# Optimization experiments

Hardware: AMD Instinct MI355X
Metric: run time of the kernel (lower is better)

## Reference

```python
import jax, jax.numpy as jnp
import numpy as np

N = 50000      # nodes
E = 800000     # edges
D_IN = 128     # embedding_in
EP = 200000    # prediction edge pairs
CONV_DIMS = [D_IN, 128, 64, 32]
LIN_DIMS = [32, 16, 8, 1]


def setup_inputs() -> dict:
    key = jax.random.key(0)
    ks = jax.random.split(key, 20)
    inp = {
        "x": jax.random.normal(ks[0], (N, D_IN), dtype=jnp.float32),
        "edge_index": jax.random.randint(ks[1], (2, E), 0, N, dtype=jnp.int64 if jax.config.jax_enable_x64 else jnp.int32),
        "pred_edges": jax.random.randint(ks[2], (EP, 2), 0, N, dtype=jnp.int64 if jax.config.jax_enable_x64 else jnp.int32),
    }
    k = 3
    for i in range(3):  # GCNConv weights [in,out] + bias (torch GCNConv has bias)
        din, dout = CONV_DIMS[i], CONV_DIMS[i + 1]
        inp[f"cw{i}"] = jax.random.normal(ks[k], (din, dout), dtype=jnp.float32) / np.sqrt(din); k += 1
        inp[f"cb{i}"] = jax.random.normal(ks[k], (dout,), dtype=jnp.float32) * 0.01; k += 1
    for i in range(3):  # Linear weights stored [in,out]
        din, dout = LIN_DIMS[i], LIN_DIMS[i + 1]
        inp[f"lw{i}"] = jax.random.normal(ks[k], (din, dout), dtype=jnp.float32) / np.sqrt(din); k += 1
        inp[f"lb{i}"] = jax.random.normal(ks[k], (dout,), dtype=jnp.float32) * 0.01; k += 1
    return inp


def gcn_conv(x, W, b, src, dst, n):
    """PyG GCNConv: D^-1/2 (A + I) D^-1/2 X W + b, deg over dst incl. self-loop."""
    h = x @ W  # [n, dout]
    deg = jax.ops.segment_sum(jnp.ones_like(dst, dtype=h.dtype), dst, num_segments=n) + 1.0
    dis = jax.lax.rsqrt(deg)  # deg >= 1 (self loop)
    msg = h[src] * (dis[src] * dis[dst])[:, None]      # gather + per-edge normalize
    out = jax.ops.segment_sum(msg, dst, num_segments=n)  # scatter-add into targets
    out = out + h * (dis * dis)[:, None]                # self-loop contribution
    return out + b


def reference(x, edge_index, pred_edges, cw0, cb0, cw1, cb1, cw2, cb2,
              lw0, lb0, lw1, lb1, lw2, lb2):
    src, dst = edge_index[0], edge_index[1]
    n = x.shape[0]
    for W, b in ((cw0, cb0), (cw1, cb1), (cw2, cb2)):
        x = jax.nn.relu(gcn_conv(x, W, b, src, dst, n))
    x = jax.nn.relu(x @ lw0 + lb0)
    x = jax.nn.relu(x @ lw1 + lb1)
    x = jax.nn.sigmoid(x @ lw2 + lb2)  # [n, 1]
    s = x[:, 0]
    # x[pred_edges] -> [EP,2,1]; mul of pair, transpose+flatten -> [EP]
    return s[pred_edges[:, 0]] * s[pred_edges[:, 1]]
```

## Files before the change

kernel.cpp:

```cpp
#include <hip/hip_runtime.h>
#include <math.h>

constexpr int NN  = 50000;
constexpr int NP  = 50048;
constexpr int NE  = 800000;
constexpr int NEP = 200000;

constexpr int NBKT  = 256;
constexpr int CAP   = 4096;
constexpr int CAPC  = 4096;
constexpr int CHUNK = 4096;

constexpr int BKB = (NE + CHUNK - 1) / CHUNK;
constexpr int W0B = 128 * 128 / 256;
constexpr int W1B = 128 * 64 / 256;
constexpr int W2B = 64 * 32 / 256;
constexpr int FRONT_BLOCKS = BKB + W0B + W1B + W2B;

constexpr int GEMM0_BLKS = NP / 64;
constexpr int NODE_BLKS32 = (NN + 31) / 32;
constexpr int NODE_BLKS16 = (NN + 15) / 16;

constexpr float M0_SCALE  = 16.0f;
constexpr float M0_ISCALE = 1.0f / 16.0f;
constexpr float M1_SCALE  = 16.0f;
constexpr float M1_ISCALE = 1.0f / 16.0f;
constexpr float M2_SCALE  = 16.0f;
constexpr float M2_ISCALE = 1.0f / 16.0f;

typedef _Float16 half8_t  __attribute__((ext_vector_type(8)));
typedef __fp16   fp16x2_t __attribute__((ext_vector_type(2)));
typedef float    float4_t __attribute__((ext_vector_type(4)));

static inline int cdiv(long long a, int b) { return (int)((a + b - 1) / b); }

static __device__ inline unsigned char f32_to_fp8(float v) {
    int p = __builtin_amdgcn_cvt_pk_fp8_f32(v, v, 0, false);
    return (unsigned char)(p & 0xFF);
}

static __device__ inline void fp8x8_acc(uint2 u, float d, float* a) {
    auto f0 = __builtin_amdgcn_cvt_pk_f32_fp8((int)u.x, false);
    auto f1 = __builtin_amdgcn_cvt_pk_f32_fp8((int)u.x, true);
    auto f2 = __builtin_amdgcn_cvt_pk_f32_fp8((int)u.y, false);
    auto f3 = __builtin_amdgcn_cvt_pk_f32_fp8((int)u.y, true);
    a[0] = fmaf(f0[0], d, a[0]); a[1] = fmaf(f0[1], d, a[1]);
    a[2] = fmaf(f1[0], d, a[2]); a[3] = fmaf(f1[1], d, a[3]);
    a[4] = fmaf(f2[0], d, a[4]); a[5] = fmaf(f2[1], d, a[5]);
    a[6] = fmaf(f3[0], d, a[6]); a[7] = fmaf(f3[1], d, a[7]);
}

static __device__ inline void fp8x8_add(uint2 u, float* a) {
    auto f0 = __builtin_amdgcn_cvt_pk_f32_fp8((int)u.x, false);
    auto f1 = __builtin_amdgcn_cvt_pk_f32_fp8((int)u.x, true);
    auto f2 = __builtin_amdgcn_cvt_pk_f32_fp8((int)u.y, false);
    auto f3 = __builtin_amdgcn_cvt_pk_f32_fp8((int)u.y, true);
    a[0] += f0[0]; a[1] += f0[1];
    a[2] += f1[0]; a[3] += f1[1];
    a[4] += f2[0]; a[5] += f2[1];
    a[6] += f3[0]; a[7] += f3[1];
}

__global__ __launch_bounds__(256) void k_front(const int* __restrict__ src,
        const int* __restrict__ dst, int* __restrict__ binCnt,
        unsigned int* __restrict__ ebuf,
        const float* __restrict__ cw0, _Float16* __restrict__ WT0,
        const float* __restrict__ cw1, _Float16* __restrict__ WT1,
        const float* __restrict__ cw2, _Float16* __restrict__ WT2) {
    const int tid = threadIdx.x;
    const int bid = blockIdx.x;

    if (bid < BKB) {
        __shared__ int hist[NBKT];
        __shared__ int base[NBKT];
        __shared__ int cur[NBKT];
        const int e0 = bid * CHUNK;
        hist[tid] = 0;
        __syncthreads();
        int  s[16], bn[16], dl[16];
        bool okq[4];
#pragma unroll
        for (int q = 0; q < 4; ++q) {
            int i = e0 + q * 1024 + tid * 4;
            bool ok = i < NE;
            okq[q] = ok;
            if (ok) {
                int4 d4 = *(const int4*)(dst + i);
                int4 s4 = *(const int4*)(src + i);
                s[q*4+0] = s4.x; bn[q*4+0] = d4.x >> 8; dl[q*4+0] = d4.x & 255;
                s[q*4+1] = s4.y; bn[q*4+1] = d4.y >> 8; dl[q*4+1] = d4.y & 255;
                s[q*4+2] = s4.z; bn[q*4+2] = d4.z >> 8; dl[q*4+2] = d4.z & 255;
                s[q*4+3] = s4.w; bn[q*4+3] = d4.w >> 8; dl[q*4+3] = d4.w & 255;
                atomicAdd(&hist[bn[q*4+0]], 1);
                atomicAdd(&hist[bn[q*4+1]], 1);
                atomicAdd(&hist[bn[q*4+2]], 1);
                atomicAdd(&hist[bn[q*4+3]], 1);
            }
        }
        __syncthreads();
        base[tid] = hist[tid] ? atomicAdd(&binCnt[tid], hist[tid]) : 0;
        cur[tid] = 0;
        __syncthreads();
#pragma unroll
        for (int q = 0; q < 4; ++q) {
            if (okq[q]) {
#pragma unroll
                for (int u = 0; u < 4; ++u) {
                    int j = q * 4 + u;
                    int slot = base[bn[j]] + atomicAdd(&cur[bn[j]], 1);
                    ebuf[bn[j] * CAP + slot] = (unsigned int)s[j] | ((unsigned int)dl[j] << 16);
                }
            }
        }
        return;
    }
    if (bid < BKB + W0B) {
        int idx = (bid - BKB) * 256 + tid;
        int k = idx >> 7, n = idx & 127;
        WT0[(size_t)n * 128 + k] = (_Float16)cw0[idx];
        return;
    }
    if (bid < BKB + W0B + W1B) {
        int idx = (bid - BKB - W0B) * 256 + tid;
        int k = idx >> 6, n = idx & 63;
        WT1[(size_t)n * 128 + k] = (_Float16)cw1[idx];
        return;
    }
    {
        int idx = (bid - BKB - W0B - W1B) * 256 + tid;
        int k = idx >> 5, n = idx & 31;
        WT2[(size_t)n * 64 + k] = (_Float16)cw2[idx];
    }
}

__global__ __launch_bounds__(256) void k_csr_gemm0(const unsigned int* __restrict__ ebuf,
        const int* __restrict__ binCnt, int* __restrict__ off, float* __restrict__ dis,
        unsigned short* __restrict__ csr,
        const float* __restrict__ X, const _Float16* __restrict__ WT,
        unsigned char* __restrict__ g, int n) {
    const int tid = threadIdx.x;
    const int bid = blockIdx.x;

    if (bid < NBKT) {
        __shared__ int hist[256];
        __shared__ int sh[256];
        __shared__ int cur[256];
        const int bin = bid;
        const int cnt = binCnt[bin];
        const unsigned int* eb = ebuf + (size_t)bin * CAP;

        hist[tid] = 0;
        __syncthreads();
        for (int i = tid; i < cnt; i += 256)
            atomicAdd(&hist[eb[i] >> 16], 1);
        __syncthreads();

        int v  = hist[tid];
        int pv = (v + 3) & ~3;
        sh[tid] = pv;
        __syncthreads();
        for (int d = 1; d < 256; d <<= 1) {
            int t = (tid >= d) ? sh[tid - d] : 0;
            __syncthreads();
            sh[tid] += t;
            __syncthreads();
        }
        int start = bin * CAPC + (sh[tid] - pv);

        int node = bin * 256 + tid;
        if (node < NN) {
            off[node] = start | (pv << 20);
            dis[node] = rsqrtf((float)v + 1.0f);
        } else if (node == NN) {
            dis[node] = 0.f;
        }
        cur[tid] = start;
        __syncthreads();

        for (int i = tid; i < cnt; i += 256) {
            unsigned int e = eb[i];
            int p = atomicAdd(&cur[e >> 16], 1);
            csr[p] = (unsigned short)(e & 0xFFFFu);
        }
        for (int k2 = v; k2 < pv; ++k2) csr[start + k2] = (unsigned short)NN;
        return;
    }

    constexpr int K = 128, DOUT = 128;
    constexpr int NC = 64, NT = 4, KT = 4, MT = 2;

    const int gb   = bid - NBKT;
    const int L    = tid & 63;
    const int w    = tid >> 6;
    const int wc   = w & 1;
    const int wr   = w >> 1;
    const int r0   = gb * 64 + wr * 32;
    const int c0   = wc * NC;
    const int quad = L >> 4;
    const int lm   = L & 15;

    float4_t acc[MT][NT];
#pragma unroll
    for (int mt = 0; mt < MT; ++mt)
#pragma unroll
        for (int nt = 0; nt < NT; ++nt) acc[mt][nt] = (float4_t){0.f, 0.f, 0.f, 0.f};

#pragma unroll
    for (int kt = 0; kt < KT; ++kt) {
        half8_t a[MT], b[NT];
#pragma unroll
        for (int mt = 0; mt < MT; ++mt) {
            const float* xr = X + (size_t)(r0 + mt * 16 + lm) * K + kt * 32 + quad * 8;
            float4 u = *(const float4*)xr;
            float4 v = *(const float4*)(xr + 4);
            union { fp16x2_t h2[4]; half8_t h8; } cv;
            cv.h2[0] = __builtin_amdgcn_cvt_pkrtz(u.x, u.y);
            cv.h2[1] = __builtin_amdgcn_cvt_pkrtz(u.z, u.w);
            cv.h2[2] = __builtin_amdgcn_cvt_pkrtz(v.x, v.y);
            cv.h2[3] = __builtin_amdgcn_cvt_pkrtz(v.z, v.w);
            a[mt] = cv.h8;
        }
#pragma unroll
        for (int nt = 0; nt < NT; ++nt)
            b[nt] = *(const half8_t*)(WT + (size_t)(c0 + nt * 16 + lm) * K + kt * 32 + quad * 8);
#pragma unroll
        for (int mt = 0; mt < MT; ++mt)
#pragma unroll
            for (int nt = 0; nt < NT; ++nt)
                acc[mt][nt] = __builtin_amdgcn_mfma_f32_16x16x32_f16(a[mt], b[nt], acc[mt][nt], 0, 0, 0);
    }

#pragma unroll
    for (int mt = 0; mt < MT; ++mt) {
        int rb = r0 + mt * 16 + quad * 4;
#pragma unroll
        for (int nt = 0; nt < NT; ++nt) {
            int c = c0 + nt * 16 + lm;
#pragma unroll
            for (int reg = 0; reg < 4; ++reg) {
                int r = rb + reg;
                if (r < n)       g[(size_t)r * DOUT + c] = f32_to_fp8(acc[mt][nt][reg] * M0_SCALE);
                else if (r == n) g[(size_t)r * DOUT + c] = 0;
            }
        }
    }
}

__global__ __launch_bounds__(256) void k_agg_gemm16(const unsigned char* __restrict__ gin,
        const float* __restrict__ dis, const float* __restrict__ bias,
        const int* __restrict__ off, const unsigned short* __restrict__ csr,
        const _Float16* __restrict__ WT, unsigned char* __restrict__ gout, int n) {
    constexpr int DIN = 128, DOUT = 64;
    constexpr int XS = DIN + 8;
    __shared__ _Float16 sX[16 * XS];

    const int tid  = threadIdx.x;
    const int l16  = tid & 15;
    const int ln   = tid >> 4;
    const int r0   = blockIdx.x * 16;
    const int node = r0 + ln;

    const uint2* gp = (const uint2*)gin;

    if (blockIdx.x == 0 && tid < DOUT / 8)
        ((uint2*)(gout + (size_t)n * DOUT))[tid] = (uint2){0u, 0u};

    float dd = dis[node];
    uint2 hv = gp[(size_t)node * 16 + l16];
    float a[8] = {0.f, 0.f, 0.f, 0.f, 0.f, 0.f, 0.f, 0.f};
    fp8x8_acc(hv, dd, a);

    int pk = off[node];
    int e0 = pk & 0xFFFFF;
    int e1 = e0 + (pk >> 20);
    int e = e0;
    for (; e + 7 < e1; e += 8) {
        ushort4 c4 = *(const ushort4*)(csr + e);
        ushort4 c8 = *(const ushort4*)(csr + e + 4);
        uint2 v0 = gp[(size_t)c4.x * 16 + l16];
        uint2 v1 = gp[(size_t)c4.y * 16 + l16];
        uint2 v2 = gp[(size_t)c4.z * 16 + l16];
        uint2 v3 = gp[(size_t)c4.w * 16 + l16];
        uint2 v4 = gp[(size_t)c8.x * 16 + l16];
        uint2 v5 = gp[(size_t)c8.y * 16 + l16];
        uint2 v6 = gp[(size_t)c8.z * 16 + l16];
        uint2 v7 = gp[(size_t)c8.w * 16 + l16];
        float d0 = dis[c4.x], d1 = dis[c4.y], d2 = dis[c4.z], d3 = dis[c4.w];
        float d4 = dis[c8.x], d5 = dis[c8.y], d6 = dis[c8.z], d7 = dis[c8.w];
        fp8x8_acc(v0, d0, a); fp8x8_acc(v1, d1, a);
        fp8x8_acc(v2, d2, a); fp8x8_acc(v3, d3, a);
        fp8x8_acc(v4, d4, a); fp8x8_acc(v5, d5, a);
        fp8x8_acc(v6, d6, a); fp8x8_acc(v7, d7, a);
    }
    if (e < e1) {
        ushort4 c4 = *(const ushort4*)(csr + e);
        uint2 v0 = gp[(size_t)c4.x * 16 + l16];
        uint2 v1 = gp[(size_t)c4.y * 16 + l16];
        uint2 v2 = gp[(size_t)c4.z * 16 + l16];
        uint2 v3 = gp[(size_t)c4.w * 16 + l16];
        float d0 = dis[c4.x], d1 = dis[c4.y], d2 = dis[c4.z], d3 = dis[c4.w];
        fp8x8_acc(v0, d0, a); fp8x8_acc(v1, d1, a);
        fp8x8_acc(v2, d2, a); fp8x8_acc(v3, d3, a);
    }
    {
        float ddp = dd * M0_ISCALE;
        half8_t o;
#pragma unroll
        for (int j = 0; j < 8; ++j)
            o[j] = (_Float16)fmaxf(fmaf(a[j], ddp, bias[l16 * 8 + j]), 0.f);
        *(half8_t*)(sX + ln * XS + l16 * 8) = o;
    }
    __syncthreads();

    const int L    = tid & 63;
    const int w    = tid >> 6;
    const int quad = L >> 4;
    const int lm   = L & 15;
    const int c0   = w * 16;

    float4_t acc = (float4_t){0.f, 0.f, 0.f, 0.f};
#pragma unroll
    for (int kt = 0; kt < DIN / 32; ++kt) {
        half8_t b  = *(const half8_t*)(WT + (size_t)(c0 + lm) * DIN + kt * 32 + quad * 8);
        half8_t aF = *(const half8_t*)(sX + lm * XS + kt * 32 + quad * 8);
        acc = __builtin_amdgcn_mfma_f32_16x16x32_f16(aF, b, acc, 0, 0, 0);
    }
    int rb = r0 + quad * 4;
    float dv[4];
    *(float4*)dv = *(const float4*)(dis + rb);
#pragma unroll
    for (int reg = 0; reg < 4; ++reg)
        gout[(size_t)(rb + reg) * DOUT + c0 + lm] = f32_to_fp8(acc[reg] * dv[reg] * M1_SCALE);
}

__global__ __launch_bounds__(256) void k_agg_gemm8(const unsigned char* __restrict__ gin,
        const float* __restrict__ dis, const float* __restrict__ bias,
        const int* __restrict__ off, const unsigned short* __restrict__ csr,
        const _Float16* __restrict__ WT, unsigned char* __restrict__ gout, int n) {
    constexpr int DIN = 64, DOUT = 32;
    constexpr int XS = DIN + 8;
    __shared__ _Float16 sX[32 * XS];

    const int tid  = threadIdx.x;
    const int l8   = tid & 7;
    const int ln   = tid >> 3;
    const int r0   = blockIdx.x * 32;
    const int node = r0 + ln;

    const uint2* gp = (const uint2*)gin;

    if (node < n) {
        float dd = dis[node];
        uint2 hv = gp[(size_t)node * 8 + l8];
        float a[8] = {0.f, 0.f, 0.f, 0.f, 0.f, 0.f, 0.f, 0.f};
        fp8x8_add(hv, a);
        int pk = off[node];
        int e0 = pk & 0xFFFFF;
        int e1 = e0 + (pk >> 20);
        int e = e0;
        for (; e + 7 < e1; e += 8) {
            ushort4 c4 = *(const ushort4*)(csr + e);
            ushort4 c8 = *(const ushort4*)(csr + e + 4);
            uint2 v0 = gp[(size_t)c4.x * 8 + l8];
            uint2 v1 = gp[(size_t)c4.y * 8 + l8];
            uint2 v2 = gp[(size_t)c4.z * 8 + l8];
            uint2 v3 = gp[(size_t)c4.w * 8 + l8];
            uint2 v4 = gp[(size_t)c8.x * 8 + l8];
            uint2 v5 = gp[(size_t)c8.y * 8 + l8];
            uint2 v6 = gp[(size_t)c8.z * 8 + l8];
            uint2 v7 = gp[(size_t)c8.w * 8 + l8];
            fp8x8_add(v0, a); fp8x8_add(v1, a);
            fp8x8_add(v2, a); fp8x8_add(v3, a);
            fp8x8_add(v4, a); fp8x8_add(v5, a);
            fp8x8_add(v6, a); fp8x8_add(v7, a);
        }
        if (e < e1) {
            ushort4 c4 = *(const ushort4*)(csr + e);
            uint2 v0 = gp[(size_t)c4.x * 8 + l8];
            uint2 v1 = gp[(size_t)c4.y * 8 + l8];
            uint2 v2 = gp[(size_t)c4.z * 8 + l8];
            uint2 v3 = gp[(size_t)c4.w * 8 + l8];
            fp8x8_add(v0, a); fp8x8_add(v1, a);
            fp8x8_add(v2, a); fp8x8_add(v3, a);
        }
        float ddp = dd * M1_ISCALE;
        half8_t o;
#pragma unroll
        for (int j = 0; j < 8; ++j)
            o[j] = (_Float16)fmaxf(fmaf(a[j], ddp, bias[l8 * 8 + j]), 0.f);
        *(half8_t*)(sX + ln * XS + l8 * 8) = o;
    } else {
        *(half8_t*)(sX + ln * XS + l8 * 8) =
            (half8_t){(_Float16)0.f, (_Float16)0.f, (_Float16)0.f, (_Float16)0.f,
                      (_Float16)0.f, (_Float16)0.f, (_Float16)0.f, (_Float16)0.f};
    }
    __syncthreads();

    const int L    = tid & 63;
    const int w    = tid >> 6;
    const int quad = L >> 4;
    const int lm   = L & 15;
    const int c0   = (w & 1) * 16;
    const int m0   = (w >> 1) * 16;

    float4_t acc = (float4_t){0.f, 0.f, 0.f, 0.f};
#pragma unroll
    for (int kt = 0; kt < DIN / 32; ++kt) {
        half8_t b  = *(const half8_t*)(WT + (size_t)(c0 + lm) * DIN + kt * 32 + quad * 8);
        half8_t aF = *(const half8_t*)(sX + (m0 + lm) * XS + kt * 32 + quad * 8);
        acc = __builtin_amdgcn_mfma_f32_16x16x32_f16(aF, b, acc, 0, 0, 0);
    }
    int rb = r0 + m0 + quad * 4;
    float dv[4];
    *(float4*)dv = *(const float4*)(dis + rb);
#pragma unroll
    for (int reg = 0; reg < 4; ++reg) {
        int r = rb + reg;
        if (r < n)       gout[(size_t)r * DOUT + c0 + lm] = f32_to_fp8(acc[reg] * dv[reg] * M2_SCALE);
        else if (r == n) gout[(size_t)r * DOUT + c0 + lm] = 0;
    }
}

__global__ __launch_bounds__(256) void k_agg_mlp(const unsigned char* __restrict__ g,
        const float* __restrict__ dis, const float* __restrict__ b,
        const int* __restrict__ off, const unsigned short* __restrict__ csr,
        const float* __restrict__ lw0, const float* __restrict__ lb0,
        const float* __restrict__ lw1, const float* __restrict__ lb1,
        const float* __restrict__ lw2, const float* __restrict__ lb2,
        float* __restrict__ sv, int n) {
    __shared__ float sh[32 * 33];
    const int tid  = threadIdx.x;
    const int l8   = tid & 7;
    const int lane = l8 & 3;
    const int grp  = l8 >> 2;
    const int ln   = tid >> 3;
    const int node = blockIdx.x * 32 + ln;

    const uint2* gp = (const uint2*)g;

    if (node < n) {
        float dd = dis[node];
        float a[8] = {0.f, 0.f, 0.f, 0.f, 0.f, 0.f, 0.f, 0.f};
        if (grp == 0) fp8x8_add(gp[(size_t)node * 4 + lane], a);
        int pk = off[node];
        int e0 = pk & 0xFFFFF;
        int e1 = e0 + (pk >> 20);
        for (int e = e0 + grp * 4; e < e1; e += 8) {
            ushort4 c4 = *(const ushort4*)(csr + e);
            uint2 v0 = gp[(size_t)c4.x * 4 + lane];
            uint2 v1 = gp[(size_t)c4.y * 4 + lane];
            uint2 v2 = gp[(size_t)c4.z * 4 + lane];
            uint2 v3 = gp[(size_t)c4.w * 4 + lane];
            fp8x8_add(v0, a); fp8x8_add(v1, a);
            fp8x8_add(v2, a); fp8x8_add(v3, a);
        }
#pragma unroll
        for (int j = 0; j < 8; ++j) a[j] += __shfl_xor(a[j], 4);
        if (grp == 0) {
            float ddp = dd * M2_ISCALE;
            float* row = sh + ln * 33 + lane * 8;
#pragma unroll
            for (int j = 0; j < 8; ++j)
                row[j] = fmaxf(fmaf(a[j], ddp, b[lane * 8 + j]), 0.f);
        }
    }
    __syncthreads();

    if (tid < 32) {
        int node2 = blockIdx.x * 32 + tid;
        if (node2 < n) {
            const float* v = sh + tid * 33;
            float a[16];
#pragma unroll
            for (int j = 0; j < 16; ++j) {
                float acc = lb0[j];
#pragma unroll
                for (int k = 0; k < 32; ++k) acc = fmaf(v[k], lw0[k * 16 + j], acc);
                a[j] = fmaxf(acc, 0.f);
            }
            float b8[8];
#pragma unroll
            for (int j = 0; j < 8; ++j) {
                float acc = lb1[j];
#pragma unroll
                for (int k = 0; k < 16; ++k) acc = fmaf(a[k], lw1[k * 8 + j], acc);
                b8[j] = fmaxf(acc, 0.f);
            }
            float z = lb2[0];
#pragma unroll
            for (int k = 0; k < 8; ++k) z = fmaf(b8[k], lw2[k], z);
            sv[node2] = 1.0f / (1.0f + expf(-z));
        }
    }
}

__global__ void k_pred(const float* __restrict__ s, const int* __restrict__ pe,
                       float* __restrict__ out, int ep2) {
    int i = blockIdx.x * blockDim.x + threadIdx.x;
    if (i >= ep2) return;
    int4 p = ((const int4*)pe)[i];
    float2 o;
    o.x = s[p.x] * s[p.y];
    o.y = s[p.z] * s[p.w];
    ((float2*)out)[i] = o;
}

extern "C" void kernel_launch(void* const* d_in, const int* in_sizes, int n_in,
                              void* d_out, int out_size, void* d_ws, size_t ws_size,
                              hipStream_t stream) {
    const float* x   = (const float*)d_in[0];
    const int*   ei  = (const int*)d_in[1];
    const int*   pe  = (const int*)d_in[2];
    const float* cw0 = (const float*)d_in[3];
    const float* cb0 = (const float*)d_in[4];
    const float* cw1 = (const float*)d_in[5];
    const float* cb1 = (const float*)d_in[6];
    const float* cw2 = (const float*)d_in[7];
    const float* cb2 = (const float*)d_in[8];
    const float* lw0 = (const float*)d_in[9];
    const float* lb0 = (const float*)d_in[10];
    const float* lw1 = (const float*)d_in[11];
    const float* lb1 = (const float*)d_in[12];
    const float* lw2 = (const float*)d_in[13];
    const float* lb2 = (const float*)d_in[14];

    const int* src = ei;
    const int* dst = ei + NE;

    char* w = (char*)d_ws;
    float*          dis  = (float*)w;           w += sizeof(float) * (NN + 16);
    unsigned char*  M0   = (unsigned char*)w;   w += (size_t)(NN + 1) * 128;
    unsigned char*  M1   = (unsigned char*)w;   w += (size_t)(NN + 1) * 64;
    unsigned char*  M2   = (unsigned char*)w;   w += (size_t)(NN + 1) * 32;
    float*          sv   = (float*)w;           w += sizeof(float) * NN;
    _Float16*       WT0  = (_Float16*)w;        w += sizeof(_Float16) * 128 * 128;
    _Float16*       WT1  = (_Float16*)w;        w += sizeof(_Float16) * 64 * 128;
    _Float16*       WT2  = (_Float16*)w;        w += sizeof(_Float16) * 32 * 64;
    int*            off  = (int*)w;             w += sizeof(int) * NN;
    unsigned short* csr  = (unsigned short*)w;  w += sizeof(unsigned short) * (size_t)NBKT * CAPC;
    int*            binCnt = (int*)w;           w += sizeof(int) * NBKT;
    unsigned int*   ebuf = (unsigned int*)w;    w += sizeof(unsigned int) * (size_t)NBKT * CAP;

    const int T = 256;

    (void)hipMemsetAsync(binCnt, 0, sizeof(int) * NBKT, stream);
    k_front<<<FRONT_BLOCKS, 256, 0, stream>>>(src, dst, binCnt, ebuf,
                                              cw0, WT0, cw1, WT1, cw2, WT2);

    k_csr_gemm0<<<NBKT + GEMM0_BLKS, 256, 0, stream>>>(ebuf, binCnt, off, dis, csr,
                                                       x, WT0, M0, NN);

    k_agg_gemm16<<<NODE_BLKS16, 256, 0, stream>>>(M0, dis, cb0,
                                                  off, csr, WT1, M1, NN);

    k_agg_gemm8<<<NODE_BLKS32, 256, 0, stream>>>(M1, dis, cb1,
                                                 off, csr, WT2, M2, NN);

    k_agg_mlp<<<NODE_BLKS32, 256, 0, stream>>>(M2, dis, cb2, off, csr,
                                               lw0, lb0, lw1, lb1, lw2, lb2, sv, NN);

    k_pred<<<cdiv(NEP / 2, T), T, 0, stream>>>(sv, pe, (float*)d_out, NEP / 2);
}
```

Baseline: 180.5 us.

## Pre-scale layer-0 features by source degree and overlap GEMM0 with CSR build via flags

The layer-0 GEMM blocks now multiply each output row by its dis value before fp8 quantization. They wait on a per-bucket release/acquire flag published by the CSR-building blocks, and they loop persistently over tiles with a fixed grid of 768 blocks. This lets the first aggregation kernel drop its per-neighbor dis gather and fma and use a plain add with wider uint4 loads, 8 lanes per node and 32 nodes per block. It removes a random dis load per edge and improves gather width, at the cost of spin-wait synchronization across blocks in the same kernel, which relies on the CSR blocks being scheduled first. The flags are cleared by widening the existing memset.

After: 234.0 us. +29.6%, slower.

```diff
diff --git a/kernel.cpp b/kernel.cpp
--- a/kernel.cpp
+++ b/kernel.cpp
@@ -17,9 +17,10 @@
 constexpr int W2B = 64 * 32 / 256;
 constexpr int FRONT_BLOCKS = BKB + W0B + W1B + W2B;
 
-constexpr int GEMM0_BLKS = NP / 64;
+constexpr int GEMM0_TILES = NP / 64;
+constexpr int GEMM0_BLKS  = 768;
 constexpr int NODE_BLKS32 = (NN + 31) / 32;
-constexpr int NODE_BLKS16 = (NN + 15) / 16;
+constexpr int NODE_BLKS64 = (NN + 63) / 64;
 
 constexpr float M0_SCALE  = 16.0f;
 constexpr float M0_ISCALE = 1.0f / 16.0f;
@@ -37,17 +38,6 @@
 static __device__ inline unsigned char f32_to_fp8(float v) {
     int p = __builtin_amdgcn_cvt_pk_fp8_f32(v, v, 0, false);
     return (unsigned char)(p & 0xFF);
-}
-
-static __device__ inline void fp8x8_acc(uint2 u, float d, float* a) {
-    auto f0 = __builtin_amdgcn_cvt_pk_f32_fp8((int)u.x, false);
-    auto f1 = __builtin_amdgcn_cvt_pk_f32_fp8((int)u.x, true);
-    auto f2 = __builtin_amdgcn_cvt_pk_f32_fp8((int)u.y, false);
-    auto f3 = __builtin_amdgcn_cvt_pk_f32_fp8((int)u.y, true);
-    a[0] = fmaf(f0[0], d, a[0]); a[1] = fmaf(f0[1], d, a[1]);
-    a[2] = fmaf(f1[0], d, a[2]); a[3] = fmaf(f1[1], d, a[3]);
-    a[4] = fmaf(f2[0], d, a[4]); a[5] = fmaf(f2[1], d, a[5]);
-    a[6] = fmaf(f3[0], d, a[6]); a[7] = fmaf(f3[1], d, a[7]);
 }
 
 static __device__ inline void fp8x8_add(uint2 u, float* a) {
@@ -59,6 +49,11 @@
     a[2] += f1[0]; a[3] += f1[1];
     a[4] += f2[0]; a[5] += f2[1];
     a[6] += f3[0]; a[7] += f3[1];
+}
+
+static __device__ inline void fp8x16_add(uint4 u, float* a) {
+    fp8x8_add((uint2){u.x, u.y}, a);
+    fp8x8_add((uint2){u.z, u.w}, a + 8);
 }
 
 __global__ __launch_bounds__(256) void k_front(const int* __restrict__ src,
@@ -133,9 +128,9 @@
     }
 }
 
-__global__ __launch_bounds__(256) void k_csr_gemm0(const unsigned int* __restrict__ ebuf,
+__global__ __launch_bounds__(256, 4) void k_csr_gemm0(const unsigned int* __restrict__ ebuf,
         const int* __restrict__ binCnt, int* __restrict__ off, float* __restrict__ dis,
-        unsigned short* __restrict__ csr,
+        unsigned short* __restrict__ csr, int* __restrict__ flag,
         const float* __restrict__ X, const _Float16* __restrict__ WT,
         unsigned char* __restrict__ g, int n) {
     const int tid = threadIdx.x;
@@ -171,11 +166,16 @@
         if (node < NN) {
             off[node] = start | (pv << 20);
             dis[node] = rsqrtf((float)v + 1.0f);
-        } else if (node == NN) {
+        } else if (node >= NN) {
             dis[node] = 0.f;
         }
         cur[tid] = start;
         __syncthreads();
+
+        if (tid == 0) {
+            __threadfence();
+            __hip_atomic_store(&flag[bin], 1, __ATOMIC_RELEASE, __HIP_MEMORY_SCOPE_AGENT);
+        }
 
         for (int i = tid; i < cnt; i += 256) {
             unsigned int e = eb[i];
@@ -189,60 +189,70 @@
     constexpr int K = 128, DOUT = 128;
     constexpr int NC = 64, NT = 4, KT = 4, MT = 2;
 
-    const int gb   = bid - NBKT;
     const int L    = tid & 63;
     const int w    = tid >> 6;
     const int wc   = w & 1;
     const int wr   = w >> 1;
-    const int r0   = gb * 64 + wr * 32;
     const int c0   = wc * NC;
     const int quad = L >> 4;
     const int lm   = L & 15;
 
-    float4_t acc[MT][NT];
-#pragma unroll
-    for (int mt = 0; mt < MT; ++mt)
-#pragma unroll
-        for (int nt = 0; nt < NT; ++nt) acc[mt][nt] = (float4_t){0.f, 0.f, 0.f, 0.f};
-
-#pragma unroll
-    for (int kt = 0; kt < KT; ++kt) {
-        half8_t a[MT], b[NT];
+    for (int t = bid - NBKT; t < GEMM0_TILES; t += GEMM0_BLKS) {
+        const int r0 = t * 64 + wr * 32;
+
+        float4_t acc[MT][NT];
+#pragma unroll
+        for (int mt = 0; mt < MT; ++mt)
+#pragma unroll
+            for (int nt = 0; nt < NT; ++nt) acc[mt][nt] = (float4_t){0.f, 0.f, 0.f, 0.f};
+
+#pragma unroll
+        for (int kt = 0; kt < KT; ++kt) {
+            half8_t a[MT], b[NT];
+#pragma unroll
+            for (int mt = 0; mt < MT; ++mt) {
+                const float* xr = X + (size_t)(r0 + mt * 16 + lm) * K + kt * 32 + quad * 8;
+                float4 u = *(const float4*)xr;
+                float4 v = *(const float4*)(xr + 4);
+                union { fp16x2_t h2[4]; half8_t h8; } cv;
+                cv.h2[0] = __builtin_amdgcn_cvt_pkrtz(u.x, u.y);
+                cv.h2[1] = __builtin_amdgcn_cvt_pkrtz(u.z, u.w);
+                cv.h2[2] = __builtin_amdgcn_cvt_pkrtz(v.x, v.y);
+                cv.h2[3] = __builtin_amdgcn_cvt_pkrtz(v.z, v.w);
+                a[mt] = cv.h8;
+            }
+#pragma unroll
+            for (int nt = 0; nt < NT; ++nt)
+                b[nt] = *(const half8_t*)(WT + (size_t)(c0 + nt * 16 + lm) * K + kt * 32 + quad * 8);
+#pragma unroll
+            for (int mt = 0; mt < MT; ++mt)
+#pragma unroll
+                for (int nt = 0; nt < NT; ++nt)
+                    acc[mt][nt] = __builtin_amdgcn_mfma_f32_16x16x32_f16(a[mt], b[nt], acc[mt][nt], 0, 0, 0);
+        }
+
+        const int bin = (t * 64) >> 8;
+        if (tid == 0)
+            while (__hip_atomic_load(&flag[bin], __ATOMIC_ACQUIRE, __HIP_MEMORY_SCOPE_AGENT) == 0) {}
+        __syncthreads();
+
 #pragma unroll
         for (int mt = 0; mt < MT; ++mt) {
-            const float* xr = X + (size_t)(r0 + mt * 16 + lm) * K + kt * 32 + quad * 8;
-            float4 u = *(const float4*)xr;
-            float4 v = *(const float4*)(xr + 4);
-            union { fp16x2_t h2[4]; half8_t h8; } cv;
-            cv.h2[0] = __builtin_amdgcn_cvt_pkrtz(u.x, u.y);
-            cv.h2[1] = __builtin_amdgcn_cvt_pkrtz(u.z, u.w);
-            cv.h2[2] = __builtin_amdgcn_cvt_pkrtz(v.x, v.y);
-            cv.h2[3] = __builtin_amdgcn_cvt_pkrtz(v.z, v.w);
-            a[mt] = cv.h8;
-        }
-#pragma unroll
-        for (int nt = 0; nt < NT; ++nt)
-            b[nt] = *(const half8_t*)(WT + (size_t)(c0 + nt * 16 + lm) * K + kt * 32 + quad * 8);
-#pragma unroll
-        for (int mt = 0; mt < MT; ++mt)
-#pragma unroll
-            for (int nt = 0; nt < NT; ++nt)
-                acc[mt][nt] = __builtin_amdgcn_mfma_f32_16x16x32_f16(a[mt], b[nt], acc[mt][nt], 0, 0, 0);
-    }
-
-#pragma unroll
-    for (int mt = 0; mt < MT; ++mt) {
-        int rb = r0 + mt * 16 + quad * 4;
-#pragma unroll
-        for (int nt = 0; nt < NT; ++nt) {
-            int c = c0 + nt * 16 + lm;
-#pragma unroll
-            for (int reg = 0; reg < 4; ++reg) {
-                int r = rb + reg;
-                if (r < n)       g[(size_t)r * DOUT + c] = f32_to_fp8(acc[mt][nt][reg] * M0_SCALE);
-                else if (r == n) g[(size_t)r * DOUT + c] = 0;
+            int rb = r0 + mt * 16 + quad * 4;
+            float dv[4];
+            *(float4*)dv = *(const float4*)(dis + rb);
+#pragma unroll
+            for (int nt = 0; nt < NT; ++nt) {
+                int c = c0 + nt * 16 + lm;
+#pragma unroll
+                for (int reg = 0; reg < 4; ++reg) {
+                    int r = rb + reg;
+                    if (r < n)       g[(size_t)r * DOUT + c] = f32_to_fp8(acc[mt][nt][reg] * dv[reg] * M0_SCALE);
+                    else if (r == n) g[(size_t)r * DOUT + c] = 0;
+                }
             }
         }
+        __syncthreads();
     }
 }
 
@@ -252,63 +262,68 @@
         const _Float16* __restrict__ WT, unsigned char* __restrict__ gout, int n) {
     constexpr int DIN = 128, DOUT = 64;
     constexpr int XS = DIN + 8;
-    __shared__ _Float16 sX[16 * XS];
+    __shared__ _Float16 sX[32 * XS];
 
     const int tid  = threadIdx.x;
-    const int l16  = tid & 15;
-    const int ln   = tid >> 4;
-    const int r0   = blockIdx.x * 16;
+    const int l8   = tid & 7;
+    const int ln   = tid >> 3;
+    const int r0   = blockIdx.x * 32;
     const int node = r0 + ln;
 
-    const uint2* gp = (const uint2*)gin;
+    const uint4* gp = (const uint4*)gin;
 
     if (blockIdx.x == 0 && tid < DOUT / 8)
         ((uint2*)(gout + (size_t)n * DOUT))[tid] = (uint2){0u, 0u};
 
-    float dd = dis[node];
-    uint2 hv = gp[(size_t)node * 16 + l16];
-    float a[8] = {0.f, 0.f, 0.f, 0.f, 0.f, 0.f, 0.f, 0.f};
-    fp8x8_acc(hv, dd, a);
-
-    int pk = off[node];
-    int e0 = pk & 0xFFFFF;
-    int e1 = e0 + (pk >> 20);
-    int e = e0;
-    for (; e + 7 < e1; e += 8) {
-        ushort4 c4 = *(const ushort4*)(csr + e);
-        ushort4 c8 = *(const ushort4*)(csr + e + 4);
-        uint2 v0 = gp[(size_t)c4.x * 16 + l16];
-        uint2 v1 = gp[(size_t)c4.y * 16 + l16];
-        uint2 v2 = gp[(size_t)c4.z * 16 + l16];
-        uint2 v3 = gp[(size_t)c4.w * 16 + l16];
-        uint2 v4 = gp[(size_t)c8.x * 16 + l16];
-        uint2 v5 = gp[(size_t)c8.y * 16 + l16];
-        uint2 v6 = gp[(size_t)c8.z * 16 + l16];
-        uint2 v7 = gp[(size_t)c8.w * 16 + l16];
-        float d0 = dis[c4.x], d1 = dis[c4.y], d2 = dis[c4.z], d3 = dis[c4.w];
-        float d4 = dis[c8.x], d5 = dis[c8.y], d6 = dis[c8.z], d7 = dis[c8.w];
-        fp8x8_acc(v0, d0, a); fp8x8_acc(v1, d1, a);
-        fp8x8_acc(v2, d2, a); fp8x8_acc(v3, d3, a);
-        fp8x8_acc(v4, d4, a); fp8x8_acc(v5, d5, a);
-        fp8x8_acc(v6, d6, a); fp8x8_acc(v7, d7, a);
-    }
-    if (e < e1) {
-        ushort4 c4 = *(const ushort4*)(csr + e);
-        uint2 v0 = gp[(size_t)c4.x * 16 + l16];
-        uint2 v1 = gp[(size_t)c4.y * 16 + l16];
-        uint2 v2 = gp[(size_t)c4.z * 16 + l16];
-        uint2 v3 = gp[(size_t)c4.w * 16 + l16];
-        float d0 = dis[c4.x], d1 = dis[c4.y], d2 = dis[c4.z], d3 = dis[c4.w];
-        fp8x8_acc(v0, d0, a); fp8x8_acc(v1, d1, a);
-        fp8x8_acc(v2, d2, a); fp8x8_acc(v3, d3, a);
-    }
-    {
+    if (node < n) {
+        float dd = dis[node];
+        uint4 hv = gp[(size_t)node * 8 + l8];
+        float a[16] = {0.f,0.f,0.f,0.f,0.f,0.f,0.f,0.f,0.f,0.f,0.f,0.f,0.f,0.f,0.f,0.f};
+        fp8x16_add(hv, a);
+
+        int pk = off[node];
+        int e0 = pk & 0xFFFFF;
+        int e1 = e0 + (pk >> 20);
+        int e = e0;
+        for (; e + 7 < e1; e += 8) {
+            ushort4 c4 = *(const ushort4*)(csr + e);
+            ushort4 c8 = *(const ushort4*)(csr + e + 4);
+            uint4 v0 = gp[(size_t)c4.x * 8 + l8];
+            uint4 v1 = gp[(size_t)c4.y * 8 + l8];
+            uint4 v2 = gp[(size_t)c4.z * 8 + l8];
+            uint4 v3 = gp[(size_t)c4.w * 8 + l8];
+            uint4 v4 = gp[(size_t)c8.x * 8 + l8];
+            uint4 v5 = gp[(size_t)c8.y * 8 + l8];
+            uint4 v6 = gp[(size_t)c8.z * 8 + l8];
+            uint4 v7 = gp[(size_t)c8.w * 8 + l8];
+            fp8x16_add(v0, a); fp8x16_add(v1, a);
+            fp8x16_add(v2, a); fp8x16_add(v3, a);
+            fp8x16_add(v4, a); fp8x16_add(v5, a);
+            fp8x16_add(v6, a); fp8x16_add(v7, a);
+        }
+        if (e < e1) {
+            ushort4 c4 = *(const ushort4*)(csr + e);
+            uint4 v0 = gp[(size_t)c4.x * 8 + l8];
+            uint4 v1 = gp[(size_t)c4.y * 8 + l8];
+            uint4 v2 = gp[(size_t)c4.z * 8 + l8];
+            uint4 v3 = gp[(size_t)c4.w * 8 + l8];
+            fp8x16_add(v0, a); fp8x16_add(v1, a);
+            fp8x16_add(v2, a); fp8x16_add(v3, a);
+        }
         float ddp = dd * M0_ISCALE;
-        half8_t o;
-#pragma unroll
-        for (int j = 0; j < 8; ++j)
-            o[j] = (_Float16)fmaxf(fmaf(a[j], ddp, bias[l16 * 8 + j]), 0.f);
-        *(half8_t*)(sX + ln * XS + l16 * 8) = o;
+        half8_t o0, o1;
+#pragma unroll
+        for (int j = 0; j < 8; ++j) {
+            o0[j] = (_Float16)fmaxf(fmaf(a[j],     ddp, bias[l8 * 16 + j]),     0.f);
+            o1[j] = (_Float16)fmaxf(fmaf(a[j + 8], ddp, bias[l8 * 16 + 8 + j]), 0.f);
+        }
+        *(half8_t*)(sX + ln * XS + l8 * 16)     = o0;
+        *(half8_t*)(sX + ln * XS + l8 * 16 + 8) = o1;
+    } else {
+        half8_t z = (half8_t){(_Float16)0.f,(_Float16)0.f,(_Float16)0.f,(_Float16)0.f,
+                              (_Float16)0.f,(_Float16)0.f,(_Float16)0.f,(_Float16)0.f};
+        *(half8_t*)(sX + ln * XS + l8 * 16)     = z;
+        *(half8_t*)(sX + ln * XS + l8 * 16 + 8) = z;
     }
     __syncthreads();
 
@@ -318,19 +333,25 @@
     const int lm   = L & 15;
     const int c0   = w * 16;
 
-    float4_t acc = (float4_t){0.f, 0.f, 0.f, 0.f};
-#pragma unroll
-    for (int kt = 0; kt < DIN / 32; ++kt) {
-        half8_t b  = *(const half8_t*)(WT + (size_t)(c0 + lm) * DIN + kt * 32 + quad * 8);
-        half8_t aF = *(const half8_t*)(sX + lm * XS + kt * 32 + quad * 8);
-        acc = __builtin_amdgcn_mfma_f32_16x16x32_f16(aF, b, acc, 0, 0, 0);
-    }
-    int rb = r0 + quad * 4;
-    float dv[4];
-    *(float4*)dv = *(const float4*)(dis + rb);
-#pragma unroll
-    for (int reg = 0; reg < 4; ++reg)
-        gout[(size_t)(rb + reg) * DOUT + c0 + lm] = f32_to_fp8(acc[reg] * dv[reg] * M1_SCALE);
+#pragma unroll
+    for (int mh = 0; mh < 2; ++mh) {
+        const int m0 = mh * 16;
+        float4_t acc = (float4_t){0.f, 0.f, 0.f, 0.f};
+#pragma unroll
+        for (int kt = 0; kt < DIN / 32; ++kt) {
+            half8_t b  = *(const half8_t*)(WT + (size_t)(c0 + lm) * DIN + kt * 32 + quad * 8);
+            half8_t aF = *(const half8_t*)(sX + (m0 + lm) * XS + kt * 32 + quad * 8);
+            acc = __builtin_amdgcn_mfma_f32_16x16x32_f16(aF, b, acc, 0, 0, 0);
+        }
+        int rb = r0 + m0 + quad * 4;
+        float dv[4];
+        *(float4*)dv = *(const float4*)(dis + rb);
+#pragma unroll
+        for (int reg = 0; reg < 4; ++reg) {
+            int r = rb + reg;
+            if (r < n) gout[(size_t)r * DOUT + c0 + lm] = f32_to_fp8(acc[reg] * dv[reg] * M1_SCALE);
+        }
+    }
 }
 
 __global__ __launch_bounds__(256) void k_agg_gemm8(const unsigned char* __restrict__ gin,
@@ -528,7 +549,7 @@
     const int* dst = ei + NE;
 
     char* w = (char*)d_ws;
-    float*          dis  = (float*)w;           w += sizeof(float) * (NN + 16);
+    float*          dis  = (float*)w;           w += sizeof(float) * (NN + 64);
     unsigned char*  M0   = (unsigned char*)w;   w += (size_t)(NN + 1) * 128;
     unsigned char*  M1   = (unsigned char*)w;   w += (size_t)(NN + 1) * 64;
     unsigned char*  M2   = (unsigned char*)w;   w += (size_t)(NN + 1) * 32;
@@ -539,18 +560,19 @@
     int*            off  = (int*)w;             w += sizeof(int) * NN;
     unsigned short* csr  = (unsigned short*)w;  w += sizeof(unsigned short) * (size_t)NBKT * CAPC;
     int*            binCnt = (int*)w;           w += sizeof(int) * NBKT;
+    int*            flag = (int*)w;             w += sizeof(int) * NBKT;
     unsigned int*   ebuf = (unsigned int*)w;    w += sizeof(unsigned int) * (size_t)NBKT * CAP;
 
     const int T = 256;
 
-    (void)hipMemsetAsync(binCnt, 0, sizeof(int) * NBKT, stream);
+    (void)hipMemsetAsync(binCnt, 0, sizeof(int) * NBKT * 2, stream);
     k_front<<<FRONT_BLOCKS, 256, 0, stream>>>(src, dst, binCnt, ebuf,
                                               cw0, WT0, cw1, WT1, cw2, WT2);
 
     k_csr_gemm0<<<NBKT + GEMM0_BLKS, 256, 0, stream>>>(ebuf, binCnt, off, dis, csr,
-                                                       x, WT0, M0, NN);
-
-    k_agg_gemm16<<<NODE_BLKS16, 256, 0, stream>>>(M0, dis, cb0,
+                                                       flag, x, WT0, M0, NN);
+
+    k_agg_gemm16<<<NODE_BLKS32, 256, 0, stream>>>(M0, dis, cb0,
                                                   off, csr, WT1, M1, NN);
 
     k_agg_gemm8<<<NODE_BLKS32, 256, 0, stream>>>(M1, dis, cb1,
```
